# Kernel tuning notes

Hardware: AMD Instinct MI355X
Metric: run time of the kernel (lower is better)

## Reference

```python
import jax, jax.numpy as jnp
import numpy as np
from jax import lax

NUM_BLOCKS = 8
BLOCK = 4  # hidden_size 32 // num_blocks 8
LAMBDA = 0.01  # sparsity_threshold
BN_EPS = 1e-5


def _bn(x, gamma, beta):
    # training-mode BatchNorm2d over (N, H, W) per channel
    mean = jnp.mean(x, axis=(0, 2, 3), keepdims=True)
    var = jnp.var(x, axis=(0, 2, 3), keepdims=True)
    return gamma[None, :, None, None] * (x - mean) * lax.rsqrt(var + BN_EPS) + beta[None, :, None, None]


def _softshrink(x, lam):
    return jnp.where(x > lam, x - lam, jnp.where(x < -lam, x + lam, jnp.zeros_like(x)))


def _afno(x, w1, b1, w2, b2):
    # AFNO2D_channelfirst: rfft2 -> block-diagonal complex 2-layer MLP -> softshrink
    # -> multiply with original spectrum -> irfft2 -> residual add
    B, C, H, W = x.shape
    bias = x
    xf = jnp.fft.rfft2(x, axes=(2, 3), norm="ortho")          # [B, C, H, W//2+1] complex
    orig = xf
    Wf = xf.shape[-1]
    xb = xf.reshape(B, NUM_BLOCKS, BLOCK, H, Wf)
    xr, xi = jnp.real(xb), jnp.imag(xb)
    # layer 1 (complex block matmul + bias + ReLU)
    o1r = jax.nn.relu(jnp.einsum('bkihw,kio->bkohw', xr, w1[0])
                      - jnp.einsum('bkihw,kio->bkohw', xi, w1[1])
                      + b1[0][None, :, :, None, None])
    o1i = jax.nn.relu(jnp.einsum('bkihw,kio->bkohw', xi, w1[0])
                      + jnp.einsum('bkihw,kio->bkohw', xr, w1[1])
                      + b1[1][None, :, :, None, None])
    # layer 2
    o2r = (jnp.einsum('bkihw,kio->bkohw', o1r, w2[0])
           - jnp.einsum('bkihw,kio->bkohw', o1i, w2[1])
           + b2[0][None, :, :, None, None])
    o2i = (jnp.einsum('bkihw,kio->bkohw', o1i, w2[0])
           + jnp.einsum('bkihw,kio->bkohw', o1r, w2[1])
           + b2[1][None, :, :, None, None])
    o2r = _softshrink(o2r, LAMBDA)
    o2i = _softshrink(o2i, LAMBDA)
    z = (o2r + 1j * o2i).reshape(B, C, H, Wf)
    z = z * orig                                              # spectral gating by original spectrum
    out = jnp.fft.irfft2(z, s=(H, W), axes=(2, 3), norm="ortho")
    return out + bias


def setup_inputs() -> dict:
    key = jax.random.key(0)
    ks = jax.random.split(key, 6)
    return {
        "x": jax.random.normal(ks[0], (4, 32, 512, 512), jnp.float32),
        "conv_w": jax.random.normal(ks[1], (32, 32, 3, 3), jnp.float32) * 0.05,
        "conv_b": jnp.zeros((32,), jnp.float32),
        "bn1_gamma": jnp.ones((32,), jnp.float32),
        "bn1_beta": jnp.zeros((32,), jnp.float32),
        "w1": jax.random.normal(ks[2], (2, NUM_BLOCKS, BLOCK, BLOCK), jnp.float32) * 0.02,
        "b1": jax.random.normal(ks[3], (2, NUM_BLOCKS, BLOCK), jnp.float32) * 0.02,
        "w2": jax.random.normal(ks[4], (2, NUM_BLOCKS, BLOCK, BLOCK), jnp.float32) * 0.02,
        "b2": jax.random.normal(ks[5], (2, NUM_BLOCKS, BLOCK), jnp.float32) * 0.02,
        "bn2_gamma": jnp.ones((32,), jnp.float32),
        "bn2_beta": jnp.zeros((32,), jnp.float32),
    }


def reference(x, conv_w, conv_b, bn1_gamma, bn1_beta, w1, b1, w2, b2, bn2_gamma, bn2_beta):
    # conv1 = Conv3x3(norm=True, act=True): conv 3x3 pad 1 + BN + ReLU
    y = lax.conv_general_dilated(x, conv_w, (1, 1), ((1, 1), (1, 1)),
                                 dimension_numbers=('NCHW', 'OIHW', 'NCHW'))
    y = y + conv_b[None, :, None, None]
    y = jax.nn.relu(_bn(y, bn1_gamma, bn1_beta))
    fo = _afno(y, w1, b1, w2, b2)
    fo = _bn(fo, bn2_gamma, bn2_beta)
    return jax.nn.relu(y + fo)
```

## Files before the change

kernel.cpp:

```cpp
#include <hip/hip_runtime.h>

#define WF 257
#define LAM 0.01f
#define ROWL 588
#define LP(i) ((i) + (((i)>>4)<<1) + (((i)>>6)<<1))

#define WSYNC() do { asm volatile("" ::: "memory"); __builtin_amdgcn_wave_barrier(); asm volatile("" ::: "memory"); } while(0)

typedef __attribute__((ext_vector_type(8))) short short8;
typedef __attribute__((ext_vector_type(4))) float f32x4;

__device__ __forceinline__ ushort f2bf(float f){
    unsigned u = __float_as_uint(f);
    unsigned r = (u + 0x7fffu + ((u >> 16) & 1u)) >> 16;
    return (ushort)r;
}
__device__ __forceinline__ float bf2f(ushort u){ return __uint_as_float((uint)u << 16); }
__device__ __forceinline__ uint packbf(float a, float b){
    return (uint)f2bf(a) | ((uint)f2bf(b) << 16);
}
__device__ __forceinline__ float2 unpackbf(uint u){
    return make_float2(__uint_as_float(u << 16), __uint_as_float(u & 0xffff0000u));
}

__device__ __forceinline__ float2 cmul(float2 a, float2 b){
    return make_float2(a.x*b.x - a.y*b.y, a.x*b.y + a.y*b.x);
}
__device__ __forceinline__ float2 cadd(float2 a, float2 b){ return make_float2(a.x+b.x, a.y+b.y); }
__device__ __forceinline__ float2 csub(float2 a, float2 b){ return make_float2(a.x-b.x, a.y-b.y); }

template<int NTHREADS>
__device__ __forceinline__ void ld_tw(float2* tw, const float2* __restrict__ twg, int tid){
    for (int t = tid; t < 256; t += NTHREADS)
        ((float4*)tw)[t] = ((const float4*)twg)[t];
}

template<bool INV>
__device__ __forceinline__ float2 twz(const float2* tw, int idx){
    float2 w = tw[idx];
    if (INV) w.y = -w.y;
    return w;
}

template<bool INV>
__device__ __forceinline__ void dft8(float2 v[8]) {
    const float R = 0.70710678118654752f;
    float2 y0=v[0], y1=v[4], y2=v[2], y3=v[6], y4=v[1], y5=v[5], y6=v[3], y7=v[7];
    float2 t;
    t=y1; y1=csub(y0,t); y0=cadd(y0,t);
    t=y3; y3=csub(y2,t); y2=cadd(y2,t);
    t=y5; y5=csub(y4,t); y4=cadd(y4,t);
    t=y7; y7=csub(y6,t); y6=cadd(y6,t);
    t=y2; y2=csub(y0,t); y0=cadd(y0,t);
    t = INV ? make_float2(-y3.y, y3.x) : make_float2(y3.y, -y3.x);
    y3=csub(y1,t); y1=cadd(y1,t);
    t=y6; y6=csub(y4,t); y4=cadd(y4,t);
    t = INV ? make_float2(-y7.y, y7.x) : make_float2(y7.y, -y7.x);
    y7=csub(y5,t); y5=cadd(y5,t);
    t=y4; y4=csub(y0,t); y0=cadd(y0,t);
    { float2 w8 = INV ? make_float2(R, R) : make_float2(R,-R);
      t=cmul(y5,w8); y5=csub(y1,t); y1=cadd(y1,t); }
    t = INV ? make_float2(-y6.y, y6.x) : make_float2(y6.y, -y6.x);
    y6=csub(y2,t); y2=cadd(y2,t);
    { float2 w8 = INV ? make_float2(-R, R) : make_float2(-R,-R);
      t=cmul(y7,w8); y7=csub(y3,t); y3=cadd(y3,t); }
    v[0]=y0; v[1]=y1; v[2]=y2; v[3]=y3; v[4]=y4; v[5]=y5; v[6]=y6; v[7]=y7;
}

__device__ __forceinline__ void oct_write(float2* drow, int l, const float2 v[8]){
    float4* p = (float4*)(drow + LP(8*l));
    p[0]=make_float4(v[0].x,v[0].y,v[1].x,v[1].y);
    p[1]=make_float4(v[2].x,v[2].y,v[3].x,v[3].y);
    p[2]=make_float4(v[4].x,v[4].y,v[5].x,v[5].y);
    p[3]=make_float4(v[6].x,v[6].y,v[7].x,v[7].y);
}

__device__ __forceinline__ void oct_gather(const float2* drow, int o0, float2 v[8]){
    const float2* b = drow + LP(o0);
    #pragma unroll
    for (int q = 0; q < 8; ++q) v[q] = b[74*q];
}

template<bool INV>
__device__ __forceinline__ void fft_wave12(float2* drow, const float2* tw, int l)
{
    WSYNC();
    {
        int a = l&7, m = l>>3;
        float2* b = drow + 74*m + a;
        float2 v[8];
        v[0] = b[0];
        v[1] = cmul(b[8],  twz<INV>(tw, 8*a));
        v[2] = cmul(b[18], twz<INV>(tw, 16*a));
        v[3] = cmul(b[26], twz<INV>(tw, 24*a));
        v[4] = cmul(b[36], twz<INV>(tw, 32*a));
        v[5] = cmul(b[44], twz<INV>(tw, 40*a));
        v[6] = cmul(b[54], twz<INV>(tw, 48*a));
        v[7] = cmul(b[62], twz<INV>(tw, 56*a));
        dft8<INV>(v);
        b[0]=v[0]; b[8]=v[1]; b[18]=v[2]; b[26]=v[3]; b[36]=v[4]; b[44]=v[5]; b[54]=v[6]; b[62]=v[7];
    }
    WSYNC();
    {
        float2* b = drow + l + 2*(l>>4);
        float2 v[8];
        v[0] = b[0];
        #pragma unroll
        for (int q = 1; q < 8; ++q)
            v[q] = cmul(b[74*q], twz<INV>(tw, (l*q)&511));
        dft8<INV>(v);
        #pragma unroll
        for (int q = 0; q < 8; ++q) b[74*q] = v[q];
    }
    WSYNC();
}

__global__ void k_twiddle(float2* __restrict__ twg){
    int t = blockIdx.x*256 + threadIdx.x;
    if (t < 512) {
        float s, c;
        sincosf((float)t * (-6.2831853071795864769f/512.0f), &s, &c);
        twg[t] = make_float2(c, s);
    }
}

__global__ void k_wprep(const float* __restrict__ w, ushort* __restrict__ wtp){
    int i = blockIdx.x*256 + threadIdx.x;
    if (i < 9216) {
        int j = i & 7, l = (i>>3) & 63, m = (i>>9) & 1, tap = i >> 10;
        int co = m*16 + (l & 15), ci = ((l>>4)&3)*8 + j;
        wtp[i] = f2bf(w[(co*32 + ci)*9 + tap]);
    }
}

__global__ __launch_bounds__(256) void k_transpose(const float* __restrict__ x, ushort* __restrict__ xt){
    __shared__ ushort tl[64][36];
    const int tid = threadIdx.x;
    const int w0 = blockIdx.x*64, h = blockIdx.y, b = blockIdx.z;
    #pragma unroll
    for (int it = 0; it < 8; ++it) {
        int i = it*256 + tid, c = i >> 6, ww = i & 63;
        tl[ww][c] = f2bf(x[(((size_t)b*32 + c)*512 + h)*512 + w0 + ww]);
    }
    __syncthreads();
    const int ww = tid >> 2, c0 = (tid & 3) * 8;
    uint4 v;
    v.x = *(const uint*)&tl[ww][c0+0];
    v.y = *(const uint*)&tl[ww][c0+2];
    v.z = *(const uint*)&tl[ww][c0+4];
    v.w = *(const uint*)&tl[ww][c0+6];
    *(uint4*)(xt + ((((size_t)b*512 + h)*512 + w0 + ww)*32 + c0)) = v;
}

__global__ __launch_bounds__(256) void k_conv_mfma(
    const ushort* __restrict__ xt, const ushort* __restrict__ wtp,
    const float* __restrict__ bias, ushort* __restrict__ out, float* __restrict__ stats)
{
    __shared__ float sred[64];
    const int tid = threadIdx.x;
    const int wid = tid >> 6, lane = tid & 63;
    const int h = blockIdx.y*4 + wid;
    const int w0 = blockIdx.x*64;
    const int b = blockIdx.z;

    short8 wa[9][2];
    #pragma unroll
    for (int tap = 0; tap < 9; ++tap)
        #pragma unroll
        for (int m = 0; m < 2; ++m)
            wa[tap][m] = *reinterpret_cast<const short8*>(wtp + ((tap*2 + m)*64 + lane)*8);

    f32x4 acc[2][4];
    #pragma unroll
    for (int m = 0; m < 2; ++m)
        #pragma unroll
        for (int n = 0; n < 4; ++n)
            acc[m][n] = (f32x4){0.f, 0.f, 0.f, 0.f};

    const int c0 = ((lane >> 4) & 3) * 8;
    const int pw = w0 + (lane & 15);
    const size_t ibase = (size_t)b * 512 * 512;

    #pragma unroll
    for (int dy = -1; dy <= 1; ++dy) {
        const int hh = h + dy;
        const bool hok = (unsigned)hh < 512u;
        #pragma unroll
        for (int dx = -1; dx <= 1; ++dx) {
            const int tap = (dy+1)*3 + (dx+1);
            short8 bfr[4];
            #pragma unroll
            for (int n = 0; n < 4; ++n) {
                const int ww = pw + n*16 + dx;
                short8 v = {0,0,0,0,0,0,0,0};
                if (hok && (unsigned)ww < 512u)
                    v = *reinterpret_cast<const short8*>(xt + ((ibase + (size_t)hh*512 + ww)*32 + c0));
                bfr[n] = v;
            }
            #pragma unroll
            for (int m = 0; m < 2; ++m)
                #pragma unroll
                for (int n = 0; n < 4; ++n)
                    acc[m][n] = __builtin_amdgcn_mfma_f32_16x16x32_bf16(wa[tap][m], bfr[n], acc[m][n], 0, 0, 0);
        }
    }

    if (tid < 64) sred[tid] = 0.f;
    __syncthreads();

    float bv[2][4];
    #pragma unroll
    for (int m = 0; m < 2; ++m)
        #pragma unroll
        for (int r = 0; r < 4; ++r)
            bv[m][r] = bias[m*16 + ((lane>>4)&3)*4 + r];

    float s8[8], q8[8];
    #pragma unroll
    for (int i = 0; i < 8; ++i) { s8[i] = 0.f; q8[i] = 0.f; }

    #pragma unroll
    for (int m = 0; m < 2; ++m) {
        #pragma unroll
        for (int n = 0; n < 4; ++n) {
            #pragma unroll
            for (int r = 0; r < 4; ++r) {
                const int co = m*16 + ((lane>>4)&3)*4 + r;
                const int ww = w0 + n*16 + (lane & 15);
                float val = acc[m][n][r] + bv[m][r];
                out[(((size_t)b*32 + co)*512 + h)*512 + ww] = f2bf(val);
                s8[m*4+r] += val;
                q8[m*4+r] += val*val;
            }
        }
    }
    #pragma unroll
    for (int i = 0; i < 8; ++i) {
        #pragma unroll
        for (int off = 1; off < 16; off <<= 1) {
            s8[i] += __shfl_xor(s8[i], off, 64);
            q8[i] += __shfl_xor(q8[i], off, 64);
        }
    }
    if ((lane & 15) == 0) {
        #pragma unroll
        for (int m = 0; m < 2; ++m)
            #pragma unroll
            for (int r = 0; r < 4; ++r) {
                const int co = m*16 + ((lane>>4)&3)*4 + r;
                atomicAdd(&sred[co], s8[m*4+r]);
                atomicAdd(&sred[32+co], q8[m*4+r]);
            }
    }
    __syncthreads();
    if (tid < 64) {
        int bin = (blockIdx.y*8 + blockIdx.x + blockIdx.z) & 63;
        atomicAdd(&stats[bin*64 + tid], sred[tid]);
    }
}

__global__ void k_finalize(const float* __restrict__ stats, int nbins, const float* __restrict__ g,
                           const float* __restrict__ bta, float* __restrict__ bnp)
{
    int c = threadIdx.x;
    if (c < 32) {
        float s = 0.f, q = 0.f;
        for (int i = 0; i < nbins; ++i) { s += stats[i*64 + c]; q += stats[i*64 + 32 + c]; }
        const float inv_n = 1.f/1048576.f;
        float mean = s * inv_n;
        float var  = q * inv_n - mean*mean;
        float sc = g[c] * rsqrtf(var + 1e-5f);
        bnp[c] = sc;
        bnp[32+c] = bta[c] - mean*sc;
    }
}

__global__ void k_finalize2(const float* __restrict__ ystats, const float* __restrict__ sstats,
                            const float* __restrict__ g, const float* __restrict__ bta,
                            float* __restrict__ bnp2)
{
    int c = threadIdx.x;
    if (c < 32) {
        float Sy = 0.f, Sy2 = 0.f, Sgg = 0.f, Sgu = 0.f, Sg0 = 0.f;
        for (int i = 0; i < 64; ++i){ Sy  += ystats[i*64 + c]; Sy2 += ystats[i*64 + 32 + c]; }
        for (int i = 0; i < 32; ++i){ Sgg += sstats[i*96 + c]; Sgu += sstats[i*96 + 32 + c]; Sg0 += sstats[i*96 + 64 + c]; }
        const float inv_n = 1.f/1048576.f;
        float Sfo  = Sg0 + Sy;
        float Sfo2 = Sgg*(1.f/512.f) + Sgu*(2.f/512.f) + Sy2;
        float mean = Sfo*inv_n;
        float var  = Sfo2*inv_n - mean*mean;
        float sc = g[c]*rsqrtf(var + 1e-5f);
        bnp2[c] = sc;
        bnp2[32+c] = bta[c] - mean*sc;
    }
}

__global__ __launch_bounds__(512) void k_rowfft_fwd(
    const ushort* __restrict__ cvo, const float* __restrict__ bnp,
    const float2* __restrict__ twg, uint* __restrict__ spec, float* __restrict__ ystats)
{
    __shared__ float2 tw[512];
    __shared__ float2 d[8*ROWL];
    const int tid = threadIdx.x;
    const int h0 = blockIdx.x * 16;
    const int bc = blockIdx.y;
    const int c = bc & 31;
    ld_tw<512>(tw, twg, tid);
    __syncthreads();
    const float s1 = bnp[c], t1 = bnp[32+c];
    const int row = tid >> 6, l = tid & 63;
    const int o0 = ((l&7)<<3) | (l>>3);
    float2* drow = d + row*ROWL;
    const ushort* rp0 = cvo + ((size_t)bc*512 + h0 + 2*row)*512 + o0;
    const ushort* rp1 = rp0 + 512;
    float ls = 0.f, lsq = 0.f;
    float2 v[8];
    #pragma unroll
    for (int q = 0; q < 8; ++q) {
        float y0 = fmaxf(fmaf(bf2f(rp0[64*q]), s1, t1), 0.f);
        float y1 = fmaxf(fmaf(bf2f(rp1[64*q]), s1, t1), 0.f);
        ls += y0 + y1; lsq += y0*y0 + y1*y1;
        v[q] = make_float2(y0, y1);
    }
    dft8<false>(v);
    oct_write(drow, l, v);
    fft_wave12<false>(drow, tw, l);
    __syncthreads();
    for (int i = tid; i < 8*WF; i += 512) {
        int p = i & 7, w = i >> 3;
        float2 Z  = d[p*ROWL + LP(w)];
        float2 Zm = d[p*ROWL + LP((512 - w) & 511)];
        float x1r = 0.5f*(Z.x + Zm.x), x1i = 0.5f*(Z.y - Zm.y);
        float x2r = 0.5f*(Z.y + Zm.y), x2i = 0.5f*(Zm.x - Z.x);
        uint2 pk;
        pk.x = packbf(x1r, x1i);
        pk.y = packbf(x2r, x2i);
        *(uint2*)(spec + ((size_t)bc*WF + w)*512 + h0 + 2*p) = pk;
    }
    #pragma unroll
    for (int off = 32; off; off >>= 1){ ls += __shfl_down(ls, off, 64); lsq += __shfl_down(lsq, off, 64); }
    if (l == 0) {
        int bin = ((blockIdx.x << 3) + row) & 63;
        atomicAdd(&ystats[bin*64 + c], ls);
        atomicAdd(&ystats[bin*64 + 32 + c], lsq);
    }
}

__global__ __launch_bounds__(256) void k_colfft(uint* __restrict__ spec,
    const float* __restrict__ w1, const float* __restrict__ b1,
    const float* __restrict__ w2, const float* __restrict__ b2,
    const float2* __restrict__ twg, float* __restrict__ sstats)
{
    __shared__ float2 tw[512];
    __shared__ float2 d[4*ROWL];
    __shared__ float wl[80];
    const int tid = threadIdx.x;
    const int w = blockIdx.x;
    const int k = blockIdx.y;
    const int b = blockIdx.z;
    ld_tw<256>(tw, twg, tid);
    if (tid < 16) {
        wl[tid]      = w1[k*16 + tid];
        wl[16 + tid] = w1[128 + k*16 + tid];
        wl[32 + tid] = w2[k*16 + tid];
        wl[48 + tid] = w2[128 + k*16 + tid];
    } else if (tid < 20) {
        int o = tid - 16;
        wl[64 + o] = b1[k*4 + o];
        wl[68 + o] = b1[32 + k*4 + o];
        wl[72 + o] = b2[k*4 + o];
        wl[76 + o] = b2[32 + k*4 + o];
    }
    __syncthreads();
    const size_t base0 = ((size_t)(b*32 + k*4)*WF + w) * 512;
    const int cc = tid >> 6, l = tid & 63;
    const int o0 = ((l&7)<<3) | (l>>3);
    float2* drow = d + cc*ROWL;
    const size_t cbase = base0 + (size_t)cc*(WF*512);
    {
        const uint* sp = spec + cbase + o0;
        float2 v[8];
        #pragma unroll
        for (int q = 0; q < 8; ++q) v[q] = unpackbf(sp[64*q]);
        dft8<false>(v);
        oct_write(drow, l, v);
    }
    fft_wave12<false>(drow, tw, l);
    __syncthreads();
    #pragma unroll
    for (int rep = 0; rep < 2; ++rep) {
        const int ph = LP(rep*256 + tid);
        float xr[4], xi[4];
        #pragma unroll
        for (int i = 0; i < 4; ++i) {
            float2 vv = d[i*ROWL + ph];
            xr[i] = vv.x * (1.f/512.f);
            xi[i] = vv.y * (1.f/512.f);
        }
        float o1r[4], o1i[4];
        #pragma unroll
        for (int o = 0; o < 4; ++o) {
            float sr = wl[64+o], si = wl[68+o];
            #pragma unroll
            for (int i = 0; i < 4; ++i) {
                float wr = wl[i*4+o], wi = wl[16 + i*4+o];
                sr += xr[i]*wr - xi[i]*wi;
                si += xi[i]*wr + xr[i]*wi;
            }
            o1r[o] = fmaxf(sr, 0.f);
            o1i[o] = fmaxf(si, 0.f);
        }
        #pragma unroll
        for (int o = 0; o < 4; ++o) {
            float sr = wl[72+o], si = wl[76+o];
            #pragma unroll
            for (int i = 0; i < 4; ++i) {
                float wr = wl[32 + i*4+o], wi = wl[48 + i*4+o];
                sr += o1r[i]*wr - o1i[i]*wi;
                si += o1i[i]*wr + o1r[i]*wi;
            }
            sr = (sr > LAM) ? sr - LAM : ((sr < -LAM) ? sr + LAM : 0.f);
            si = (si > LAM) ? si - LAM : ((si < -LAM) ? si + LAM : 0.f);
            d[o*ROWL + ph] = make_float2(sr*xr[o] - si*xi[o], sr*xi[o] + si*xr[o]);
        }
    }
    __syncthreads();
    {
        float2 v[8];
        oct_gather(drow, o0, v);
        dft8<true>(v);
        WSYNC();
        oct_write(drow, l, v);
    }
    fft_wave12<true>(drow, tw, l);
    const bool edge = (w == 0) || (w == 256);
    float fgg = 0.f, fgu = 0.f, fg0 = 0.f;
    #pragma unroll
    for (int it = 0; it < 4; ++it) {
        const int pos = it*64 + l;
        uint2 up = *(const uint2*)(spec + cbase + 2*pos);
        float2 u0 = unpackbf(up.x), u1 = unpackbf(up.y);
        float4 vv = *(const float4*)(drow + LP(2*pos));
        uint2 gp;
        gp.x = packbf(vv.x, vv.y);
        gp.y = packbf(vv.z, vv.w);
        *(uint2*)(spec + cbase + 2*pos) = gp;
        float2 g0 = unpackbf(gp.x), g1 = unpackbf(gp.y);
        if (edge) {
            fgg += g0.x*g0.x + g1.x*g1.x;
            fgu += g0.x*u0.x + g1.x*u1.x;
            if (w == 0) fg0 += g0.x + g1.x;
        } else {
            fgg += 2.f*(g0.x*g0.x + g0.y*g0.y + g1.x*g1.x + g1.y*g1.y);
            fgu += 2.f*(g0.x*u0.x + g0.y*u0.y + g1.x*u1.x + g1.y*u1.y);
        }
    }
    #pragma unroll
    for (int off = 32; off; off >>= 1){
        fgg += __shfl_down(fgg, off, 64);
        fgu += __shfl_down(fgu, off, 64);
        fg0 += __shfl_down(fg0, off, 64);
    }
    if (l == 0) {
        int bin = (w + b*8 + k) & 31;
        atomicAdd(&sstats[bin*96 + k*4 + cc], fgg);
        atomicAdd(&sstats[bin*96 + 32 + k*4 + cc], fgu);
        if (w == 0) atomicAdd(&sstats[bin*96 + 64 + k*4 + cc], fg0);
    }
}

__global__ __launch_bounds__(512) void k_rowfft_inv(
    const uint* __restrict__ spec, const ushort* __restrict__ cvo,
    const float* __restrict__ bnp, const float* __restrict__ bnp2,
    const float2* __restrict__ twg, float* __restrict__ out)
{
    __shared__ float2 tw[512];
    __shared__ float2 d[8*ROWL];
    const int tid = threadIdx.x;
    const int h0 = blockIdx.x * 16;
    const int bc = blockIdx.y;
    const int c = bc & 31;
    ld_tw<512>(tw, twg, tid);
    for (int i = tid; i < 8*WF; i += 512) {
        int p = i & 7, w = i >> 3;
        uint2 pk = *(const uint2*)(spec + ((size_t)bc*WF + w)*512 + h0 + 2*p);
        float2 X1 = unpackbf(pk.x), X2 = unpackbf(pk.y);
        if (w == 0 || w == 256) { X1.y = 0.f; X2.y = 0.f; }
        d[p*ROWL + LP(w)] = make_float2(X1.x - X2.y, X1.y + X2.x);
        if ((unsigned)(w - 1) < 255u)
            d[p*ROWL + LP(512 - w)] = make_float2(X1.x + X2.y, X2.x - X1.y);
    }
    __syncthreads();
    const int row = tid >> 6, l = tid & 63;
    const int o0 = ((l&7)<<3) | (l>>3);
    float2* drow = d + row*ROWL;
    {
        float2 v[8];
        oct_gather(drow, o0, v);
        dft8<true>(v);
        WSYNC();
        oct_write(drow, l, v);
    }
    fft_wave12<true>(drow, tw, l);
    const float s1 = bnp[c],  t1 = bnp[32+c];
    const float s2 = bnp2[c], t2 = bnp2[32+c];
    const size_t gbase = ((size_t)bc*512 + h0 + 2*row)*512;
    #pragma unroll
    for (int q = 0; q < 8; ++q) {
        const int col = q*64 + l;
        float2 v = drow[LP(col)];
        float y0 = fmaxf(fmaf(bf2f(cvo[gbase + col]), s1, t1), 0.f);
        float fo0 = fmaf(v.x, (1.f/512.f), y0);
        out[gbase + col] = fmaxf(y0 + fmaf(fo0, s2, t2), 0.f);
        float y1 = fmaxf(fmaf(bf2f(cvo[gbase + 512 + col]), s1, t1), 0.f);
        float fo1 = fmaf(v.y, (1.f/512.f), y1);
        out[gbase + 512 + col] = fmaxf(y1 + fmaf(fo1, s2, t2), 0.f);
    }
}

extern "C" void kernel_launch(void* const* d_in, const int* in_sizes, int n_in,
                              void* d_out, int out_size, void* d_ws, size_t ws_size,
                              hipStream_t stream)
{
    const float* x      = (const float*)d_in[0];
    const float* conv_w = (const float*)d_in[1];
    const float* conv_b = (const float*)d_in[2];
    const float* bn1g   = (const float*)d_in[3];
    const float* bn1b   = (const float*)d_in[4];
    const float* w1     = (const float*)d_in[5];
    const float* b1     = (const float*)d_in[6];
    const float* w2     = (const float*)d_in[7];
    const float* b2     = (const float*)d_in[8];
    const float* bn2g   = (const float*)d_in[9];
    const float* bn2b   = (const float*)d_in[10];
    float* out = (float*)d_out;

    char* ws = (char*)d_ws;
    uint*   spec  = (uint*)ws;
    ushort* xt    = (ushort*)ws;
    ushort* cvo   = (ushort*)(ws + 67371008);
    ushort* wtp   = (ushort*)(ws + 67371008 + 67108864);
    float*  stats = (float*)(ws + 67371008 + 67108864 + 18432);
    float* stats1 = stats;
    float* ystats = stats + 4096;
    float* sstats = stats + 8192;
    float* bnp1   = stats + 11264;
    float* bnp2   = stats + 11328;
    float2* twg   = (float2*)(stats + 11392);

    hipMemsetAsync(stats, 0, 11264*sizeof(float), stream);
    k_twiddle<<<2, 256, 0, stream>>>(twg);
    k_wprep<<<36, 256, 0, stream>>>(conv_w, wtp);
    k_transpose<<<dim3(8,512,4), 256, 0, stream>>>(x, xt);
    k_conv_mfma<<<dim3(8,128,4), 256, 0, stream>>>(xt, wtp, conv_b, cvo, stats1);
    k_finalize<<<1, 64, 0, stream>>>(stats1, 64, bn1g, bn1b, bnp1);
    k_rowfft_fwd<<<dim3(32,128), 512, 0, stream>>>(cvo, bnp1, twg, spec, ystats);
    k_colfft<<<dim3(257,8,4), 256, 0, stream>>>(spec, w1, b1, w2, b2, twg, sstats);
    k_finalize2<<<1, 64, 0, stream>>>(ystats, sstats, bn2g, bn2b, bnp2);
    k_rowfft_inv<<<dim3(32,128), 512, 0, stream>>>(spec, cvo, bnp1, bnp2, twg, out);
}
```

Before: 350.1 us.

## Store FFT shared-memory staging as packed fp16 with simpler padding

Shared-memory FFT buffers in the row and column FFT kernels now hold each complex value as packed fp16 (one uint) instead of float2, with a new padding scheme (4 words every 64). The 1/512 normalisation moves earlier, before values are stored, so the fp16 range stays bounded. This halves LDS footprint and traffic and may raise occupancy. In exchange it adds pack/unpack conversions and loses precision in intermediate FFT stages.

```diff
diff --git a/kernel.cpp b/kernel.cpp
--- a/kernel.cpp
+++ b/kernel.cpp
@@ -2,13 +2,14 @@
 
 #define WF 257
 #define LAM 0.01f
-#define ROWL 588
-#define LP(i) ((i) + (((i)>>4)<<1) + (((i)>>6)<<1))
+#define ROWH 540
+#define LPH(i) ((i) + (((i)>>6)<<2))
 
 #define WSYNC() do { asm volatile("" ::: "memory"); __builtin_amdgcn_wave_barrier(); asm volatile("" ::: "memory"); } while(0)
 
 typedef __attribute__((ext_vector_type(8))) short short8;
 typedef __attribute__((ext_vector_type(4))) float f32x4;
+typedef __attribute__((ext_vector_type(2))) __fp16 h2v;
 
 __device__ __forceinline__ ushort f2bf(float f){
     unsigned u = __float_as_uint(f);
@@ -21,6 +22,15 @@
 }
 __device__ __forceinline__ float2 unpackbf(uint u){
     return make_float2(__uint_as_float(u << 16), __uint_as_float(u & 0xffff0000u));
+}
+__device__ __forceinline__ uint packh(float a, float b){
+    h2v h = __builtin_amdgcn_cvt_pkrtz(a, b);
+    return *(uint*)&h;
+}
+__device__ __forceinline__ uint packh2(float2 v){ return packh(v.x, v.y); }
+__device__ __forceinline__ float2 unph(uint u){
+    h2v h = *(h2v*)&u;
+    return make_float2((float)h[0], (float)h[1]);
 }
 
 __device__ __forceinline__ float2 cmul(float2 a, float2 b){
@@ -67,50 +77,45 @@
     v[0]=y0; v[1]=y1; v[2]=y2; v[3]=y3; v[4]=y4; v[5]=y5; v[6]=y6; v[7]=y7;
 }
 
-__device__ __forceinline__ void oct_write(float2* drow, int l, const float2 v[8]){
-    float4* p = (float4*)(drow + LP(8*l));
-    p[0]=make_float4(v[0].x,v[0].y,v[1].x,v[1].y);
-    p[1]=make_float4(v[2].x,v[2].y,v[3].x,v[3].y);
-    p[2]=make_float4(v[4].x,v[4].y,v[5].x,v[5].y);
-    p[3]=make_float4(v[6].x,v[6].y,v[7].x,v[7].y);
-}
-
-__device__ __forceinline__ void oct_gather(const float2* drow, int o0, float2 v[8]){
-    const float2* b = drow + LP(o0);
-    #pragma unroll
-    for (int q = 0; q < 8; ++q) v[q] = b[74*q];
+__device__ __forceinline__ void oct_write(uint* drow, int l, const float2 v[8]){
+    uint* p = drow + LPH(8*l);
+    *(uint4*)p       = make_uint4(packh2(v[0]), packh2(v[1]), packh2(v[2]), packh2(v[3]));
+    *(uint4*)(p + 4) = make_uint4(packh2(v[4]), packh2(v[5]), packh2(v[6]), packh2(v[7]));
+}
+
+__device__ __forceinline__ void oct_gather(const uint* drow, int o0, float2 v[8]){
+    const uint* b = drow + LPH(o0);
+    #pragma unroll
+    for (int q = 0; q < 8; ++q) v[q] = unph(b[68*q]);
 }
 
 template<bool INV>
-__device__ __forceinline__ void fft_wave12(float2* drow, const float2* tw, int l)
+__device__ __forceinline__ void fft_wave12(uint* drow, const float2* tw, int l)
 {
     WSYNC();
     {
         int a = l&7, m = l>>3;
-        float2* b = drow + 74*m + a;
+        uint* b = drow + 68*m + a;
         float2 v[8];
-        v[0] = b[0];
-        v[1] = cmul(b[8],  twz<INV>(tw, 8*a));
-        v[2] = cmul(b[18], twz<INV>(tw, 16*a));
-        v[3] = cmul(b[26], twz<INV>(tw, 24*a));
-        v[4] = cmul(b[36], twz<INV>(tw, 32*a));
-        v[5] = cmul(b[44], twz<INV>(tw, 40*a));
-        v[6] = cmul(b[54], twz<INV>(tw, 48*a));
-        v[7] = cmul(b[62], twz<INV>(tw, 56*a));
+        v[0] = unph(b[0]);
+        #pragma unroll
+        for (int j = 1; j < 8; ++j)
+            v[j] = cmul(unph(b[8*j]), twz<INV>(tw, 8*a*j));
         dft8<INV>(v);
-        b[0]=v[0]; b[8]=v[1]; b[18]=v[2]; b[26]=v[3]; b[36]=v[4]; b[44]=v[5]; b[54]=v[6]; b[62]=v[7];
+        #pragma unroll
+        for (int j = 0; j < 8; ++j) b[8*j] = packh2(v[j]);
     }
     WSYNC();
     {
-        float2* b = drow + l + 2*(l>>4);
+        uint* b = drow + l;
         float2 v[8];
-        v[0] = b[0];
+        v[0] = unph(b[0]);
         #pragma unroll
         for (int q = 1; q < 8; ++q)
-            v[q] = cmul(b[74*q], twz<INV>(tw, (l*q)&511));
+            v[q] = cmul(unph(b[68*q]), twz<INV>(tw, (l*q)&511));
         dft8<INV>(v);
         #pragma unroll
-        for (int q = 0; q < 8; ++q) b[74*q] = v[q];
+        for (int q = 0; q < 8; ++q) b[68*q] = packh2(v[q]);
     }
     WSYNC();
 }
@@ -300,7 +305,7 @@
     const float2* __restrict__ twg, uint* __restrict__ spec, float* __restrict__ ystats)
 {
     __shared__ float2 tw[512];
-    __shared__ float2 d[8*ROWL];
+    __shared__ uint d[8*ROWH];
     const int tid = threadIdx.x;
     const int h0 = blockIdx.x * 16;
     const int bc = blockIdx.y;
@@ -310,7 +315,7 @@
     const float s1 = bnp[c], t1 = bnp[32+c];
     const int row = tid >> 6, l = tid & 63;
     const int o0 = ((l&7)<<3) | (l>>3);
-    float2* drow = d + row*ROWL;
+    uint* drow = d + row*ROWH;
     const ushort* rp0 = cvo + ((size_t)bc*512 + h0 + 2*row)*512 + o0;
     const ushort* rp1 = rp0 + 512;
     float ls = 0.f, lsq = 0.f;
@@ -328,8 +333,8 @@
     __syncthreads();
     for (int i = tid; i < 8*WF; i += 512) {
         int p = i & 7, w = i >> 3;
-        float2 Z  = d[p*ROWL + LP(w)];
-        float2 Zm = d[p*ROWL + LP((512 - w) & 511)];
+        float2 Z  = unph(d[p*ROWH + LPH(w)]);
+        float2 Zm = unph(d[p*ROWH + LPH((512 - w) & 511)]);
         float x1r = 0.5f*(Z.x + Zm.x), x1i = 0.5f*(Z.y - Zm.y);
         float x2r = 0.5f*(Z.y + Zm.y), x2i = 0.5f*(Zm.x - Z.x);
         uint2 pk;
@@ -352,7 +357,7 @@
     const float2* __restrict__ twg, float* __restrict__ sstats)
 {
     __shared__ float2 tw[512];
-    __shared__ float2 d[4*ROWL];
+    __shared__ uint d[4*ROWH];
     __shared__ float wl[80];
     const int tid = threadIdx.x;
     const int w = blockIdx.x;
@@ -375,13 +380,16 @@
     const size_t base0 = ((size_t)(b*32 + k*4)*WF + w) * 512;
     const int cc = tid >> 6, l = tid & 63;
     const int o0 = ((l&7)<<3) | (l>>3);
-    float2* drow = d + cc*ROWL;
+    uint* drow = d + cc*ROWH;
     const size_t cbase = base0 + (size_t)cc*(WF*512);
     {
         const uint* sp = spec + cbase + o0;
         float2 v[8];
         #pragma unroll
-        for (int q = 0; q < 8; ++q) v[q] = unpackbf(sp[64*q]);
+        for (int q = 0; q < 8; ++q) {
+            float2 u = unpackbf(sp[64*q]);
+            v[q] = make_float2(u.x*(1.f/512.f), u.y*(1.f/512.f));
+        }
         dft8<false>(v);
         oct_write(drow, l, v);
     }
@@ -389,13 +397,13 @@
     __syncthreads();
     #pragma unroll
     for (int rep = 0; rep < 2; ++rep) {
-        const int ph = LP(rep*256 + tid);
+        const int ph = LPH(rep*256 + tid);
         float xr[4], xi[4];
         #pragma unroll
         for (int i = 0; i < 4; ++i) {
-            float2 vv = d[i*ROWL + ph];
-            xr[i] = vv.x * (1.f/512.f);
-            xi[i] = vv.y * (1.f/512.f);
+            float2 vv = unph(d[i*ROWH + ph]);
+            xr[i] = vv.x;
+            xi[i] = vv.y;
         }
         float o1r[4], o1i[4];
         #pragma unroll
@@ -421,7 +429,7 @@
             }
             sr = (sr > LAM) ? sr - LAM : ((sr < -LAM) ? sr + LAM : 0.f);
             si = (si > LAM) ? si - LAM : ((si < -LAM) ? si + LAM : 0.f);
-            d[o*ROWL + ph] = make_float2(sr*xr[o] - si*xi[o], sr*xi[o] + si*xr[o]);
+            d[o*ROWH + ph] = packh(sr*xr[o] - si*xi[o], sr*xi[o] + si*xr[o]);
         }
     }
     __syncthreads();
@@ -440,10 +448,11 @@
         const int pos = it*64 + l;
         uint2 up = *(const uint2*)(spec + cbase + 2*pos);
         float2 u0 = unpackbf(up.x), u1 = unpackbf(up.y);
-        float4 vv = *(const float4*)(drow + LP(2*pos));
+        uint2 dv = *(const uint2*)(drow + LPH(2*pos));
+        float2 z0 = unph(dv.x), z1 = unph(dv.y);
         uint2 gp;
-        gp.x = packbf(vv.x, vv.y);
-        gp.y = packbf(vv.z, vv.w);
+        gp.x = packbf(z0.x, z0.y);
+        gp.y = packbf(z1.x, z1.y);
         *(uint2*)(spec + cbase + 2*pos) = gp;
         float2 g0 = unpackbf(gp.x), g1 = unpackbf(gp.y);
         if (edge) {
@@ -475,7 +484,7 @@
     const float2* __restrict__ twg, float* __restrict__ out)
 {
     __shared__ float2 tw[512];
-    __shared__ float2 d[8*ROWL];
+    __shared__ uint d[8*ROWH];
     const int tid = threadIdx.x;
     const int h0 = blockIdx.x * 16;
     const int bc = blockIdx.y;
@@ -486,14 +495,15 @@
         uint2 pk = *(const uint2*)(spec + ((size_t)bc*WF + w)*512 + h0 + 2*p);
         float2 X1 = unpackbf(pk.x), X2 = unpackbf(pk.y);
         if (w == 0 || w == 256) { X1.y = 0.f; X2.y = 0.f; }
-        d[p*ROWL + LP(w)] = make_float2(X1.x - X2.y, X1.y + X2.x);
+        const float s = 1.f/512.f;
+        d[p*ROWH + LPH(w)] = packh((X1.x - X2.y)*s, (X1.y + X2.x)*s);
         if ((unsigned)(w - 1) < 255u)
-            d[p*ROWL + LP(512 - w)] = make_float2(X1.x + X2.y, X2.x - X1.y);
+            d[p*ROWH + LPH(512 - w)] = packh((X1.x + X2.y)*s, (X2.x - X1.y)*s);
     }
     __syncthreads();
     const int row = tid >> 6, l = tid & 63;
     const int o0 = ((l&7)<<3) | (l>>3);
-    float2* drow = d + row*ROWL;
+    uint* drow = d + row*ROWH;
     {
         float2 v[8];
         oct_gather(drow, o0, v);
@@ -508,12 +518,12 @@
     #pragma unroll
     for (int q = 0; q < 8; ++q) {
         const int col = q*64 + l;
-        float2 v = drow[LP(col)];
+        float2 v = unph(drow[LPH(col)]);
         float y0 = fmaxf(fmaf(bf2f(cvo[gbase + col]), s1, t1), 0.f);
-        float fo0 = fmaf(v.x, (1.f/512.f), y0);
+        float fo0 = v.x + y0;
         out[gbase + col] = fmaxf(y0 + fmaf(fo0, s2, t2), 0.f);
         float y1 = fmaxf(fmaf(bf2f(cvo[gbase + 512 + col]), s1, t1), 0.f);
-        float fo1 = fmaf(v.y, (1.f/512.f), y1);
+        float fo1 = v.y + y1;
         out[gbase + 512 + col] = fmaxf(y1 + fmaf(fo1, s2, t2), 0.f);
     }
 }
@@ -548,7 +558,7 @@
     float* bnp2   = stats + 11328;
     float2* twg   = (float2*)(stats + 11392);
 
-    hipMemsetAsync(stats, 0, 11264*sizeof(float), stream);
+    (void)hipMemsetAsync(stats, 0, 11264*sizeof(float), stream);
     k_twiddle<<<2, 256, 0, stream>>>(twg);
     k_wprep<<<36, 256, 0, stream>>>(conv_w, wtp);
     k_transpose<<<dim3(8,512,4), 256, 0, stream>>>(x, xt);
```

Result: faster. 337.6 us (-3.6%).
